# Kernel tuning notes

Hardware: AMD Instinct MI355X
Metric: run time of the kernel (lower is better)

## Reference

```python
import jax, jax.numpy as jnp
import numpy as np

N = 50000      # nodes
E = 800000     # edges (before self-loops)
G = 64         # graphs in batch
IN, HID, OUT, H = 128, 64, 64, 4
NEG_SLOPE = 0.2
BN_EPS = 1e-5


def setup_inputs() -> dict:
    key = jax.random.key(0)
    ks = jax.random.split(key, 16)
    s = 0.1
    return {
        "x": jax.random.normal(ks[0], (N, IN), jnp.float32),
        "edge_index": jax.random.randint(ks[1], (2, E), 0, N, dtype=jnp.int64),
        "batch": jnp.sort(jax.random.randint(ks[2], (N,), 0, G, dtype=jnp.int64)),
        "num_graphs": G,
        "W1": jax.random.normal(ks[3], (IN, H * HID), jnp.float32) * s,
        "att_src1": jax.random.normal(ks[4], (H, HID), jnp.float32) * s,
        "att_dst1": jax.random.normal(ks[5], (H, HID), jnp.float32) * s,
        "b1": jnp.zeros((HID,), jnp.float32),
        "W2": jax.random.normal(ks[6], (HID, H * OUT), jnp.float32) * s,
        "att_src2": jax.random.normal(ks[7], (H, OUT), jnp.float32) * s,
        "att_dst2": jax.random.normal(ks[8], (H, OUT), jnp.float32) * s,
        "b2": jnp.zeros((OUT,), jnp.float32),
        "gate_w1": jax.random.normal(ks[9], (OUT, OUT), jnp.float32) * s,
        "gate_b1": jnp.zeros((OUT,), jnp.float32),
        "bn_gamma": jnp.ones((OUT,), jnp.float32),
        "bn_beta": jnp.zeros((OUT,), jnp.float32),
        "gate_w2": jax.random.normal(ks[10], (OUT, 1), jnp.float32) * s,
        "gate_b2": jnp.zeros((1,), jnp.float32),
        "lin_w": jax.random.normal(ks[11], (OUT, 1), jnp.float32) * s,
        "lin_b": jnp.zeros((1,), jnp.float32),
    }


def segment_softmax(e, seg, num_segments):
    # numerically stable softmax over segments (per-destination / per-graph)
    m = jax.ops.segment_max(e, seg, num_segments=num_segments)
    m = jnp.where(jnp.isfinite(m), m, 0.0)
    ex = jnp.exp(e - m[seg])
    den = jax.ops.segment_sum(ex, seg, num_segments=num_segments)
    return ex / (den[seg] + 1e-16)


def gat_conv(x, src, dst, n, W, a_src, a_dst, b, heads, ch):
    h = (x @ W).reshape(n, heads, ch)                 # [N,H,C]
    asrc = jnp.sum(h * a_src, axis=-1)                # [N,H]
    adst = jnp.sum(h * a_dst, axis=-1)                # [N,H]
    e = jax.nn.leaky_relu(asrc[src] + adst[dst], NEG_SLOPE)   # [E',H]
    alpha = segment_softmax(e, dst, n)                # softmax over incoming edges
    out = jax.ops.segment_sum(h[src] * alpha[:, :, None], dst, num_segments=n)
    return jnp.mean(out, axis=1) + b                  # concat=False -> head mean


def reference(x, edge_index, batch, num_graphs, W1, att_src1, att_dst1, b1,
              W2, att_src2, att_dst2, b2, gate_w1, gate_b1, bn_gamma, bn_beta,
              gate_w2, gate_b2, lin_w, lin_b):
    n = x.shape[0]
    loop = jnp.arange(n, dtype=edge_index.dtype)      # PyG add_self_loops default
    src = jnp.concatenate([edge_index[0], loop])
    dst = jnp.concatenate([edge_index[1], loop])

    out = jax.nn.sigmoid(gat_conv(x, src, dst, n, W1, att_src1, att_dst1, b1, H, HID))
    out = jax.nn.sigmoid(gat_conv(out, src, dst, n, W2, att_src2, att_dst2, b2, H, OUT))

    # GlobalAttention pooling; gate_nn = Linear -> BN(eval, rm=0, rv=1) -> ReLU -> Linear
    g = out @ gate_w1 + gate_b1
    g = (g / jnp.sqrt(1.0 + BN_EPS)) * bn_gamma + bn_beta
    g = jax.nn.relu(g) @ gate_w2 + gate_b2            # [N,1]
    gate = segment_softmax(g, batch, num_graphs)      # per-graph softmax
    pooled = jax.ops.segment_sum(gate * out, batch, num_segments=num_graphs)  # [G,OUT]

    return jax.nn.sigmoid(pooled @ lin_w + lin_b)     # [G,1]
```

## Files before the change

### kernel.cpp

```cpp
#include <hip/hip_runtime.h>


constexpr int NN = 50000;
constexpr int EE = 800000;
constexpr int NG = 64;
constexpr float NEG = 0.2f;
constexpr int MT = NN / 16;
constexpr int SLOTS = 64;
constexpr int CH = 16;
constexpr int GB = (MT + 3) / 4;

constexpr int EB_EDGES = 4096;
constexpr int EBN = (EE + EB_EDGES - 1) / EB_EDGES;
constexpr int NBKT = (NN + 255) / 256;
constexpr int CAP = 48;
constexpr int OVFCAP = 8192;

using bf16x8 = __attribute__((ext_vector_type(8))) __bf16;
using f32x4  = __attribute__((ext_vector_type(4))) float;
using f32x2  = __attribute__((ext_vector_type(2))) float;

__device__ __forceinline__ float wred(float v) {
#pragma unroll
  for (int o = 32; o; o >>= 1) v += __shfl_down(v, o);
  return v;
}
__device__ __forceinline__ float sigmoidf(float v) { return 1.f / (1.f + __expf(-v)); }
__device__ __forceinline__ float lrelu(float v) { return fmaxf(v, NEG * v); }
__device__ __forceinline__ unsigned short f2b(float f) {
  union { float f; unsigned u; } v; v.f = f;
  unsigned r = v.u + 0x7fff + ((v.u >> 16) & 1);
  return (unsigned short)(r >> 16);
}
__device__ __forceinline__ float b2f(unsigned short b) {
  union { unsigned u; float f; } v; v.u = ((unsigned)b) << 16;
  return v.f;
}

__global__ void prep_kernel(const float* __restrict__ W1, const float* __restrict__ W2,
                            const float* __restrict__ gw1, const float* __restrict__ gamma,
                            const int* __restrict__ batch,
                            unsigned short* __restrict__ W1b, unsigned short* __restrict__ W2b,
                            unsigned short* __restrict__ Bg, int* __restrict__ goffs,
                            int* __restrict__ ovf_cnt) {
  int b = blockIdx.x;
  if (b < 128) {
    int idx = b * 256 + threadIdx.x;
    int j = idx & 7, lane = (idx >> 3) & 63, rest = idx >> 9;
    int kc = rest & 3, ntile = rest >> 2;
    W1b[idx] = f2b(W1[(kc * 32 + (lane >> 4) * 8 + j) * 256 + ntile * 16 + (lane & 15)]);
    return;
  }
  if (b < 192) {
    int idx = (b - 128) * 256 + threadIdx.x;
    int j = idx & 7, lane = (idx >> 3) & 63, rest = idx >> 9;
    int kc = rest & 1, ntile = rest >> 1;
    W2b[idx] = f2b(W2[(kc * 32 + (lane >> 4) * 8 + j) * 256 + ntile * 16 + (lane & 15)]);
    return;
  }
  if (b < 208) {
    int idx = (b - 192) * 256 + threadIdx.x;
    int j = idx & 7, lane = (idx >> 3) & 63, rest = idx >> 9;
    int kc = rest & 1, nt = rest >> 1;
    int k = kc * 32 + (lane >> 4) * 8 + j;
    int n = nt * 16 + (lane & 15);
    Bg[idx] = f2b(gw1[k * 64 + n] * gamma[n] * rsqrtf(1.f + 1e-5f));
    return;
  }
  if (threadIdx.x == 0) *ovf_cnt = 0;
  int g = threadIdx.x;
  if (g <= NG) {
    int lo = 0, hi = NN;
    while (lo < hi) {
      int mid = (lo + hi) >> 1;
      if (batch[mid] < g) lo = mid + 1; else hi = mid;
    }
    goffs[g] = lo;
  }
}

template <int K, bool A32>
__device__ __forceinline__ void gemm_body(int mt, int lane,
                                          const void* __restrict__ A_raw,
                                          const unsigned short* __restrict__ Bp,
                                          unsigned char* __restrict__ C8,
                                          const float* __restrict__ att_s,
                                          const float* __restrict__ att_d,
                                          float* __restrict__ asrc,
                                          float* __restrict__ adst) {
  constexpr int KC = K / 32;
  int m0 = mt * 16;
  int q = lane >> 4, r = lane & 15;
  f32x4 acc[16] = {};
#pragma unroll
  for (int kc = 0; kc < KC; ++kc) {
    bf16x8 a;
    if constexpr (A32) {
      const float* Arow = (const float*)A_raw + (size_t)(m0 + r) * K + q * 8 + kc * 32;
      float4 f0 = *(const float4*)Arow;
      float4 f1 = *(const float4*)(Arow + 4);
      union { bf16x8 v; unsigned short s[8]; } u;
      u.s[0] = f2b(f0.x); u.s[1] = f2b(f0.y); u.s[2] = f2b(f0.z); u.s[3] = f2b(f0.w);
      u.s[4] = f2b(f1.x); u.s[5] = f2b(f1.y); u.s[6] = f2b(f1.z); u.s[7] = f2b(f1.w);
      a = u.v;
    } else {
      a = *(const bf16x8*)((const unsigned short*)A_raw +
                           (size_t)(m0 + r) * K + q * 8 + kc * 32);
    }
#pragma unroll
    for (int nt = 0; nt < 16; ++nt) {
      bf16x8 b = *(const bf16x8*)&Bp[(((size_t)nt * KC + kc) * 64 + lane) * 8];
      acc[nt] = __builtin_amdgcn_mfma_f32_16x16x32_bf16(a, b, acc[nt], 0, 0, 0);
    }
  }
#pragma unroll
  for (int nt = 0; nt < 16; ++nt) {
    unsigned col = nt * 16 + r;
#pragma unroll
    for (int reg = 0; reg < 4; ++reg) {
      unsigned row = m0 + q * 4 + reg;
      int p = __builtin_amdgcn_cvt_pk_fp8_f32(acc[nt][reg], 0.f, 0, false);
      C8[row * 256u + col] = (unsigned char)(p & 0xff);
    }
  }
  float ps[4][4] = {}, pd[4][4] = {};
#pragma unroll
  for (int head = 0; head < 4; ++head) {
#pragma unroll
    for (int i = 0; i < 4; ++i) {
      float sv = att_s[head * 64 + i * 16 + r];
      float dv = att_d[head * 64 + i * 16 + r];
#pragma unroll
      for (int reg = 0; reg < 4; ++reg) {
        ps[head][reg] += acc[head * 4 + i][reg] * sv;
        pd[head][reg] += acc[head * 4 + i][reg] * dv;
      }
    }
  }
#pragma unroll
  for (int head = 0; head < 4; ++head)
#pragma unroll
    for (int reg = 0; reg < 4; ++reg)
#pragma unroll
      for (int o = 1; o < 16; o <<= 1) {
        ps[head][reg] += __shfl_xor(ps[head][reg], o);
        pd[head][reg] += __shfl_xor(pd[head][reg], o);
      }
  if (r == 0) {
#pragma unroll
    for (int reg = 0; reg < 4; ++reg) {
      int row = m0 + q * 4 + reg;
#pragma unroll
      for (int head = 0; head < 4; ++head) {
        asrc[row * 4 + head] = ps[head][reg];
        adst[row * 4 + head] = pd[head][reg];
      }
    }
  }
}

__global__ void gemm1_build_kernel(const float* __restrict__ x,
                                   const unsigned short* __restrict__ W1b,
                                   unsigned char* __restrict__ C8,
                                   const float* __restrict__ att_s,
                                   const float* __restrict__ att_d,
                                   float* __restrict__ asrc, float* __restrict__ adst,
                                   const int* __restrict__ ei,
                                   unsigned* __restrict__ bins,
                                   int* __restrict__ binCnt,
                                   int* __restrict__ ovf_cnt,
                                   unsigned* __restrict__ ovf) {
  int b = blockIdx.x;
  if (b < GB) {
    int wave = threadIdx.x >> 6, lane = threadIdx.x & 63;
    int mt = b * 4 + wave;
    if (mt >= MT) return;
    gemm_body<128, true>(mt, lane, x, W1b, C8, att_s, att_d, asrc, adst);
    return;
  }
  int hb = b - GB;
  __shared__ int hist[NBKT];
  for (int t = threadIdx.x; t < NBKT; t += 256) hist[t] = 0;
  __syncthreads();
  int e0 = hb * EB_EDGES + threadIdx.x * 16;
#pragma unroll
  for (int k4 = 0; k4 < 4; ++k4) {
    int e = e0 + k4 * 4;
    if (e >= EE) break;
    int4 s4 = *(const int4*)&ei[e];
    int4 d4 = *(const int4*)&ei[EE + e];
    int ss[4] = {s4.x, s4.y, s4.z, s4.w};
    int dd[4] = {d4.x, d4.y, d4.z, d4.w};
#pragma unroll
    for (int u = 0; u < 4; ++u) {
      if (e + u >= EE) break;
      int src = ss[u], dst = dd[u];
      int bkt = dst >> 8;
      int r = atomicAdd(&hist[bkt], 1);
      if (r < CAP) {
        bins[((unsigned)hb * NBKT + bkt) * CAP + r] =
            (unsigned)src | ((unsigned)(dst & 255) << 16);
      } else {
        int o = atomicAdd(ovf_cnt, 1);
        if (o < OVFCAP) ovf[o] = (unsigned)src | ((unsigned)dst << 16);
      }
    }
  }
  __syncthreads();
  for (int t = threadIdx.x; t < NBKT; t += 256) binCnt[hb * NBKT + t] = hist[t];
}

__global__ __launch_bounds__(1024) void csr_build_kernel(
    const unsigned* __restrict__ bins, const int* __restrict__ binCnt,
    const int* __restrict__ ovf_cnt, const unsigned* __restrict__ ovf,
    unsigned short* __restrict__ csr16, int* __restrict__ cnt) {
  int b = blockIdx.x;
  __shared__ int hist[256];
  int t = threadIdx.x;
  int node0 = b << 8;
  if (t < 256) {
    hist[t] = 1;
    int node = node0 + t;
    if (node < NN) csr16[(unsigned)node * SLOTS] = (unsigned short)node;
  }
  __syncthreads();
  int wave = t >> 6, lane = t & 63;
  for (int i = wave; i < EBN; i += 16) {
    int c = binCnt[i * NBKT + b];
    if (c > CAP) c = CAP;
    for (int base = 0; base < c; base += 64) {
      int j = base + lane;
      if (j < c) {
        unsigned p = bins[((unsigned)i * NBKT + b) * CAP + j];
        int dl = p >> 16, src = p & 0xffff;
        int r = atomicAdd(&hist[dl], 1);
        if (r < SLOTS) csr16[(unsigned)(node0 + dl) * SLOTS + r] = (unsigned short)src;
      }
    }
  }
  __syncthreads();
  int oc = *ovf_cnt;
  if (oc > OVFCAP) oc = OVFCAP;
  for (int j = t; j < oc; j += 1024) {
    unsigned p = ovf[j];
    int dst = (int)(p >> 16);
    if ((dst >> 8) == b) {
      int r = atomicAdd(&hist[dst & 255], 1);
      if (r < SLOTS) csr16[(unsigned)dst * SLOTS + r] = (unsigned short)(p & 0xffff);
    }
  }
  __syncthreads();
  if (t < 256) {
    int node = node0 + t;
    if (node < NN) cnt[node] = hist[t];
  }
}

__global__ void aggregate_kernel(const unsigned char* __restrict__ h8,
                                 const float* __restrict__ asrc,
                                 const float* __restrict__ adst,
                                 const int* __restrict__ cnt,
                                 const unsigned short* __restrict__ csr_src,
                                 const float* __restrict__ bias,
                                 unsigned short* __restrict__ outb) {
  int wave = threadIdx.x >> 6, lane = threadIdx.x & 63;
  int node = blockIdx.x * 4 + wave;
  if (node >= NN) return;
  int deg = min(cnt[node], SLOTS);
  int hgrp = lane >> 4;
  int hb = lane & 48;
  float adh = adst[node * 4 + hgrp];
  int src_all = csr_src[(unsigned)node * SLOTS + lane];
  float wreg[4];
  float den = 0.f;
#pragma unroll
  for (int i = 0; i < 4; ++i) {
    int slot = i * 16 + (lane & 15);
    int s = __shfl(src_all, slot);
    bool valid = slot < deg;
    float xv = asrc[(unsigned)(valid ? s : 0) * 4 + hgrp];
    float w = __expf(lrelu(xv + adh));
    wreg[i] = valid ? w : 0.f;
    den += wreg[i];
  }
#pragma unroll
  for (int o = 1; o < 16; o <<= 1) den += __shfl_xor(den, o);
  const unsigned char* hp = h8 + (unsigned)lane * 4;
  f32x2 a01 = {0.f, 0.f}, a23 = {0.f, 0.f};
  int e = 0;
#pragma unroll
  for (int i = 0; i < 4; ++i) {
    if (e >= deg) break;
    float wcur = wreg[i];
    int bound = min(deg, (i + 1) * 16);
    for (; e + 3 < bound; e += 4) {
      int s0 = __shfl(src_all, e),     s1 = __shfl(src_all, e + 1);
      int s2 = __shfl(src_all, e + 2), s3 = __shfl(src_all, e + 3);
      float w0 = __shfl(wcur, ((e)     & 15) | hb);
      float w1 = __shfl(wcur, ((e + 1) & 15) | hb);
      float w2 = __shfl(wcur, ((e + 2) & 15) | hb);
      float w3 = __shfl(wcur, ((e + 3) & 15) | hb);
      unsigned d0 = *(const unsigned*)(hp + ((unsigned)s0 << 8));
      unsigned d1 = *(const unsigned*)(hp + ((unsigned)s1 << 8));
      unsigned d2 = *(const unsigned*)(hp + ((unsigned)s2 << 8));
      unsigned d3 = *(const unsigned*)(hp + ((unsigned)s3 << 8));
      f32x2 l0 = __builtin_amdgcn_cvt_pk_f32_fp8(d0, false), u0 = __builtin_amdgcn_cvt_pk_f32_fp8(d0, true);
      f32x2 l1 = __builtin_amdgcn_cvt_pk_f32_fp8(d1, false), u1 = __builtin_amdgcn_cvt_pk_f32_fp8(d1, true);
      f32x2 l2 = __builtin_amdgcn_cvt_pk_f32_fp8(d2, false), u2 = __builtin_amdgcn_cvt_pk_f32_fp8(d2, true);
      f32x2 l3 = __builtin_amdgcn_cvt_pk_f32_fp8(d3, false), u3 = __builtin_amdgcn_cvt_pk_f32_fp8(d3, true);
      a01 += l0 * w0; a23 += u0 * w0;
      a01 += l1 * w1; a23 += u1 * w1;
      a01 += l2 * w2; a23 += u2 * w2;
      a01 += l3 * w3; a23 += u3 * w3;
    }
    for (; e < bound; ++e) {
      int s0 = __shfl(src_all, e);
      float w0 = __shfl(wcur, (e & 15) | hb);
      unsigned d0 = *(const unsigned*)(hp + ((unsigned)s0 << 8));
      f32x2 l0 = __builtin_amdgcn_cvt_pk_f32_fp8(d0, false), u0 = __builtin_amdgcn_cvt_pk_f32_fp8(d0, true);
      a01 += l0 * w0; a23 += u0 * w0;
    }
  }
  float inv = 1.f / (den + 1e-16f);
  float r0 = a01.x * inv, r1 = a01.y * inv, r2 = a23.x * inv, r3 = a23.y * inv;
  r0 += __shfl_xor(r0, 16); r0 += __shfl_xor(r0, 32);
  r1 += __shfl_xor(r1, 16); r1 += __shfl_xor(r1, 32);
  r2 += __shfl_xor(r2, 16); r2 += __shfl_xor(r2, 32);
  r3 += __shfl_xor(r3, 16); r3 += __shfl_xor(r3, 32);
  if (lane < 16) {
    float4 bv = *(const float4*)&bias[lane * 4];
    ushort4 o;
    o.x = f2b(sigmoidf(0.25f * r0 + bv.x));
    o.y = f2b(sigmoidf(0.25f * r1 + bv.y));
    o.z = f2b(sigmoidf(0.25f * r2 + bv.z));
    o.w = f2b(sigmoidf(0.25f * r3 + bv.w));
    *(ushort4*)&outb[(size_t)node * 64 + lane * 4] = o;
  }
}

__global__ void gemm2_kernel(const unsigned short* __restrict__ out1b,
                             const unsigned short* __restrict__ W2b,
                             unsigned char* __restrict__ C8,
                             const float* __restrict__ att_s,
                             const float* __restrict__ att_d,
                             float* __restrict__ asrc, float* __restrict__ adst) {
  int wave = threadIdx.x >> 6, lane = threadIdx.x & 63;
  int mt = blockIdx.x * 4 + wave;
  if (mt >= MT) return;
  gemm_body<64, false>(mt, lane, out1b, W2b, C8, att_s, att_d, asrc, adst);
}

__global__ void pool_partial_kernel(const int* __restrict__ goffs,
                                    const unsigned short* __restrict__ out2b,
                                    const unsigned short* __restrict__ Bg,
                                    const float* __restrict__ gb1,
                                    const float* __restrict__ gamma,
                                    const float* __restrict__ beta,
                                    const float* __restrict__ gw2,
                                    const float* __restrict__ gb2,
                                    float* __restrict__ part_acc,
                                    float* __restrict__ part_den) {
  int b = blockIdx.x, j = blockIdx.y;
  int beg = goffs[b], end = goffs[b + 1];
  int chunk = (end - beg + CH - 1) / CH;
  int cb = beg + j * chunk;
  int ce = min(end, cb + chunk);
  int lane = threadIdx.x & 63, wave = threadIdx.x >> 6;
  int q = lane >> 4, r = lane & 15;
  const float s = rsqrtf(1.f + 1e-5f);
  float gb2v = gb2[0];
  float accv = 0.f, den = 0.f;
  for (int n0 = cb + wave * 16; n0 < ce; n0 += 64) {
    f32x4 acc[4] = {};
    int row = n0 + r;
    if (row >= NN) row = NN - 1;
    const unsigned short* Arow = out2b + (size_t)row * 64 + q * 8;
#pragma unroll
    for (int kc = 0; kc < 2; ++kc) {
      bf16x8 a = *(const bf16x8*)(Arow + kc * 32);
#pragma unroll
      for (int nt = 0; nt < 4; ++nt) {
        bf16x8 b8 = *(const bf16x8*)&Bg[(((size_t)nt * 2 + kc) * 64 + lane) * 8];
        acc[nt] = __builtin_amdgcn_mfma_f32_16x16x32_bf16(a, b8, acc[nt], 0, 0, 0);
      }
    }
    float sum[4] = {0.f, 0.f, 0.f, 0.f};
#pragma unroll
    for (int nt = 0; nt < 4; ++nt) {
      int col = nt * 16 + r;
      float off = gb1[col] * gamma[col] * s + beta[col];
      float w2 = gw2[col];
#pragma unroll
      for (int reg = 0; reg < 4; ++reg)
        sum[reg] += fmaxf(acc[nt][reg] + off, 0.f) * w2;
    }
#pragma unroll
    for (int reg = 0; reg < 4; ++reg)
#pragma unroll
      for (int o = 1; o < 16; o <<= 1) sum[reg] += __shfl_xor(sum[reg], o);
    float gx[4];
#pragma unroll
    for (int reg = 0; reg < 4; ++reg) {
      int n = n0 + q * 4 + reg;
      gx[reg] = (n < ce) ? __expf(sum[reg] + gb2v) : 0.f;
    }
#pragma unroll
    for (int t = 0; t < 16; ++t) {
      int n = n0 + t;
      if (n >= ce) break;
      float gv = __shfl(gx[t & 3], (t >> 2) << 4);
      accv += gv * b2f(out2b[(size_t)n * 64 + lane]);
      den += gv;
    }
  }
  __shared__ float sacc[4][64];
  __shared__ float sden[4];
  sacc[wave][lane] = accv;
  if (lane == 0) sden[wave] = den;
  __syncthreads();
  if (wave == 0) {
    float a = sacc[0][lane] + sacc[1][lane] + sacc[2][lane] + sacc[3][lane];
    part_acc[((size_t)b * CH + j) * 64 + lane] = a;
    if (lane == 0) part_den[b * CH + j] = sden[0] + sden[1] + sden[2] + sden[3];
  }
}

__global__ void pool_final_kernel(const float* __restrict__ part_acc,
                                  const float* __restrict__ part_den,
                                  const float* __restrict__ lw, const float* __restrict__ lb,
                                  float* __restrict__ out) {
  int b = blockIdx.x, lane = threadIdx.x;
  float a = 0.f;
#pragma unroll
  for (int j = 0; j < CH; ++j) a += part_acc[((size_t)b * CH + j) * 64 + lane];
  float den = (lane < CH) ? part_den[b * CH + lane] : 0.f;
  den = wred(den);
  den = __shfl(den, 0);
  float p = a / (den + 1e-16f);
  float v = wred(p * lw[lane]);
  if (lane == 0) out[b] = sigmoidf(v + lb[0]);
}

extern "C" void kernel_launch(void* const* d_in, const int* in_sizes, int n_in,
                              void* d_out, int out_size, void* d_ws, size_t ws_size,
                              hipStream_t stream) {
  const float* x    = (const float*)d_in[0];
  const int*   ei   = (const int*)d_in[1];
  const int*   batch= (const int*)d_in[2];
  const float* W1   = (const float*)d_in[4];
  const float* as1  = (const float*)d_in[5];
  const float* ad1  = (const float*)d_in[6];
  const float* b1   = (const float*)d_in[7];
  const float* W2   = (const float*)d_in[8];
  const float* as2  = (const float*)d_in[9];
  const float* ad2  = (const float*)d_in[10];
  const float* b2   = (const float*)d_in[11];
  const float* gw1  = (const float*)d_in[12];
  const float* gb1  = (const float*)d_in[13];
  const float* gamma= (const float*)d_in[14];
  const float* beta = (const float*)d_in[15];
  const float* gw2  = (const float*)d_in[16];
  const float* gb2  = (const float*)d_in[17];
  const float* lw   = (const float*)d_in[18];
  const float* lb   = (const float*)d_in[19];
  float* out = (float*)d_out;

  char* ws = (char*)d_ws;
  size_t off = 0;
  auto alloc = [&](size_t bytes) -> void* {
    void* p = ws + off;
    off = (off + bytes + 255) & ~(size_t)255;
    return p;
  };
  unsigned short* W1b    = (unsigned short*)alloc((size_t)128 * 256 * 2);
  unsigned short* W2b    = (unsigned short*)alloc((size_t)64 * 256 * 2);
  unsigned short* Bg     = (unsigned short*)alloc((size_t)64 * 64 * 2);
  unsigned char*  h8     = (unsigned char*)alloc((size_t)NN * 256);
  unsigned short* out1b  = (unsigned short*)alloc((size_t)NN * 64 * 2);
  unsigned short* out2b  = (unsigned short*)alloc((size_t)NN * 64 * 2);
  float*    asrc    = (float*)alloc((size_t)NN * 4 * 4);
  float*    adst    = (float*)alloc((size_t)NN * 4 * 4);
  int*      cnt     = (int*)alloc((size_t)NN * 4);
  unsigned short* csr16 = (unsigned short*)alloc((size_t)NN * SLOTS * 2);
  unsigned* bins    = (unsigned*)alloc((size_t)EBN * NBKT * CAP * 4);
  int*      binCnt  = (int*)alloc((size_t)EBN * NBKT * 4);
  int*      ovf_cnt = (int*)alloc(256);
  unsigned* ovf     = (unsigned*)alloc((size_t)OVFCAP * 4);
  int*      goffs   = (int*)alloc((size_t)(NG + 1) * 4);
  float*    pacc    = (float*)alloc((size_t)NG * CH * 64 * 4);
  float*    pden    = (float*)alloc((size_t)NG * CH * 4);

  const int nodeBlocks = (NN + 3) / 4;

  prep_kernel<<<209, 256, 0, stream>>>(W1, W2, gw1, gamma, batch,
                                       W1b, W2b, Bg, goffs, ovf_cnt);

  gemm1_build_kernel<<<GB + EBN, 256, 0, stream>>>(x, W1b, h8, as1, ad1, asrc, adst,
                                                   ei, bins, binCnt, ovf_cnt, ovf);
  csr_build_kernel<<<NBKT, 1024, 0, stream>>>(bins, binCnt, ovf_cnt, ovf, csr16, cnt);

  aggregate_kernel<<<nodeBlocks, 256, 0, stream>>>(h8, asrc, adst, cnt, csr16, b1, out1b);

  gemm2_kernel<<<GB, 256, 0, stream>>>(out1b, W2b, h8, as2, ad2, asrc, adst);
  aggregate_kernel<<<nodeBlocks, 256, 0, stream>>>(h8, asrc, adst, cnt, csr16, b2, out2b);

  pool_partial_kernel<<<dim3(NG, CH), 256, 0, stream>>>(goffs, out2b, Bg, gb1, gamma, beta,
                                                        gw2, gb2, pacc, pden);
  pool_final_kernel<<<NG, 64, 0, stream>>>(pacc, pden, lw, lb, out);
}
```

Before: 257.1 us.

## Gather 16-byte fp8 rows per lane across four edges with LDS reduction

Reworks the GAT aggregation kernel so each group of 16 lanes loads a full 256-byte fp8 neighbour row with 16-byte vector loads. The four lane quarters each process a different edge at the same time, instead of every lane loading 4 bytes per edge in sequence. Partial sums are combined across quarters and heads through a shared-memory reduction behind a block barrier, and each lane writes one output channel. The aim is fewer, wider gather loads and more memory-level parallelism, at the cost of more accumulator registers, LDS traffic and a __syncthreads. The early-exit guard is removed on the assumption that the node count divides by 4.

Result: faster. 248.8 us (-3.2%).

```diff
diff --git a/kernel.cpp b/kernel.cpp
--- a/kernel.cpp
+++ b/kernel.cpp
@@ -15,6 +15,8 @@
 constexpr int NBKT = (NN + 255) / 256;
 constexpr int CAP = 48;
 constexpr int OVFCAP = 8192;
+
+static_assert(NN % 4 == 0, "aggregate barrier assumes no early-exit waves");
 
 using bf16x8 = __attribute__((ext_vector_type(8))) __bf16;
 using f32x4  = __attribute__((ext_vector_type(4))) float;
@@ -265,17 +267,18 @@
                                  unsigned short* __restrict__ outb) {
   int wave = threadIdx.x >> 6, lane = threadIdx.x & 63;
   int node = blockIdx.x * 4 + wave;
-  if (node >= NN) return;
   int deg = min(cnt[node], SLOTS);
   int hgrp = lane >> 4;
-  int hb = lane & 48;
+  int q4 = lane >> 4;
+  int r16 = lane & 15;
+  int hbase = (r16 >> 2) << 4;
   float adh = adst[node * 4 + hgrp];
   int src_all = csr_src[(unsigned)node * SLOTS + lane];
   float wreg[4];
   float den = 0.f;
 #pragma unroll
   for (int i = 0; i < 4; ++i) {
-    int slot = i * 16 + (lane & 15);
+    int slot = i * 16 + r16;
     int s = __shfl(src_all, slot);
     bool valid = slot < deg;
     float xv = asrc[(unsigned)(valid ? s : 0) * 4 + hgrp];
@@ -285,57 +288,78 @@
   }
 #pragma unroll
   for (int o = 1; o < 16; o <<= 1) den += __shfl_xor(den, o);
-  const unsigned char* hp = h8 + (unsigned)lane * 4;
-  f32x2 a01 = {0.f, 0.f}, a23 = {0.f, 0.f};
+
+  const unsigned char* hp = h8 + (unsigned)r16 * 16;
+  f32x2 a[8] = {};
+#define ACC4(d, wv)                                                         \
+  {                                                                         \
+    a[0] += __builtin_amdgcn_cvt_pk_f32_fp8((d).x, false) * (wv);           \
+    a[1] += __builtin_amdgcn_cvt_pk_f32_fp8((d).x, true) * (wv);            \
+    a[2] += __builtin_amdgcn_cvt_pk_f32_fp8((d).y, false) * (wv);           \
+    a[3] += __builtin_amdgcn_cvt_pk_f32_fp8((d).y, true) * (wv);            \
+    a[4] += __builtin_amdgcn_cvt_pk_f32_fp8((d).z, false) * (wv);           \
+    a[5] += __builtin_amdgcn_cvt_pk_f32_fp8((d).z, true) * (wv);            \
+    a[6] += __builtin_amdgcn_cvt_pk_f32_fp8((d).w, false) * (wv);           \
+    a[7] += __builtin_amdgcn_cvt_pk_f32_fp8((d).w, true) * (wv);            \
+  }
   int e = 0;
 #pragma unroll
   for (int i = 0; i < 4; ++i) {
     if (e >= deg) break;
     float wcur = wreg[i];
     int bound = min(deg, (i + 1) * 16);
-    for (; e + 3 < bound; e += 4) {
-      int s0 = __shfl(src_all, e),     s1 = __shfl(src_all, e + 1);
-      int s2 = __shfl(src_all, e + 2), s3 = __shfl(src_all, e + 3);
-      float w0 = __shfl(wcur, ((e)     & 15) | hb);
-      float w1 = __shfl(wcur, ((e + 1) & 15) | hb);
-      float w2 = __shfl(wcur, ((e + 2) & 15) | hb);
-      float w3 = __shfl(wcur, ((e + 3) & 15) | hb);
-      unsigned d0 = *(const unsigned*)(hp + ((unsigned)s0 << 8));
-      unsigned d1 = *(const unsigned*)(hp + ((unsigned)s1 << 8));
-      unsigned d2 = *(const unsigned*)(hp + ((unsigned)s2 << 8));
-      unsigned d3 = *(const unsigned*)(hp + ((unsigned)s3 << 8));
-      f32x2 l0 = __builtin_amdgcn_cvt_pk_f32_fp8(d0, false), u0 = __builtin_amdgcn_cvt_pk_f32_fp8(d0, true);
-      f32x2 l1 = __builtin_amdgcn_cvt_pk_f32_fp8(d1, false), u1 = __builtin_amdgcn_cvt_pk_f32_fp8(d1, true);
-      f32x2 l2 = __builtin_amdgcn_cvt_pk_f32_fp8(d2, false), u2 = __builtin_amdgcn_cvt_pk_f32_fp8(d2, true);
-      f32x2 l3 = __builtin_amdgcn_cvt_pk_f32_fp8(d3, false), u3 = __builtin_amdgcn_cvt_pk_f32_fp8(d3, true);
-      a01 += l0 * w0; a23 += u0 * w0;
-      a01 += l1 * w1; a23 += u1 * w1;
-      a01 += l2 * w2; a23 += u2 * w2;
-      a01 += l3 * w3; a23 += u3 * w3;
-    }
-    for (; e < bound; ++e) {
-      int s0 = __shfl(src_all, e);
-      float w0 = __shfl(wcur, (e & 15) | hb);
-      unsigned d0 = *(const unsigned*)(hp + ((unsigned)s0 << 8));
-      f32x2 l0 = __builtin_amdgcn_cvt_pk_f32_fp8(d0, false), u0 = __builtin_amdgcn_cvt_pk_f32_fp8(d0, true);
-      a01 += l0 * w0; a23 += u0 * w0;
-    }
-  }
-  float inv = 1.f / (den + 1e-16f);
-  float r0 = a01.x * inv, r1 = a01.y * inv, r2 = a23.x * inv, r3 = a23.y * inv;
-  r0 += __shfl_xor(r0, 16); r0 += __shfl_xor(r0, 32);
-  r1 += __shfl_xor(r1, 16); r1 += __shfl_xor(r1, 32);
-  r2 += __shfl_xor(r2, 16); r2 += __shfl_xor(r2, 32);
-  r3 += __shfl_xor(r3, 16); r3 += __shfl_xor(r3, 32);
-  if (lane < 16) {
-    float4 bv = *(const float4*)&bias[lane * 4];
-    ushort4 o;
-    o.x = f2b(sigmoidf(0.25f * r0 + bv.x));
-    o.y = f2b(sigmoidf(0.25f * r1 + bv.y));
-    o.z = f2b(sigmoidf(0.25f * r2 + bv.z));
-    o.w = f2b(sigmoidf(0.25f * r3 + bv.w));
-    *(ushort4*)&outb[(size_t)node * 64 + lane * 4] = o;
-  }
+    if (bound - e == 16) {
+      int eq = e + q4, wq = hbase + q4;
+      int s0 = __shfl(src_all, eq);
+      int s1 = __shfl(src_all, eq + 4);
+      int s2 = __shfl(src_all, eq + 8);
+      int s3 = __shfl(src_all, eq + 12);
+      float w0 = __shfl(wcur, wq);
+      float w1 = __shfl(wcur, wq + 4);
+      float w2 = __shfl(wcur, wq + 8);
+      float w3 = __shfl(wcur, wq + 12);
+      uint4 d0 = *(const uint4*)(hp + ((unsigned)s0 << 8));
+      uint4 d1 = *(const uint4*)(hp + ((unsigned)s1 << 8));
+      uint4 d2 = *(const uint4*)(hp + ((unsigned)s2 << 8));
+      uint4 d3 = *(const uint4*)(hp + ((unsigned)s3 << 8));
+      ACC4(d0, w0); ACC4(d1, w1); ACC4(d2, w2); ACC4(d3, w3);
+      e += 16;
+    } else {
+      for (; e < bound; e += 4) {
+        int gg = min(4, bound - e);
+        int q4e = min(q4, gg - 1);
+        int su = __shfl(src_all, e + q4e);
+        float wv = __shfl(wcur, hbase + (e & 15) + q4e);
+        if (q4 >= gg) wv = 0.f;
+        uint4 d = *(const uint4*)(hp + ((unsigned)su << 8));
+        ACC4(d, wv);
+      }
+    }
+  }
+#undef ACC4
+  float den2 = __shfl(den, (r16 >> 2) << 4);
+  float inv = 0.25f / (den2 + 1e-16f);
+  __shared__ float red[4][1024];
+  float* wb = &red[wave][(unsigned)lane * 16];
+  f32x4 v0 = {a[0].x * inv, a[0].y * inv, a[1].x * inv, a[1].y * inv};
+  f32x4 v1 = {a[2].x * inv, a[2].y * inv, a[3].x * inv, a[3].y * inv};
+  f32x4 v2 = {a[4].x * inv, a[4].y * inv, a[5].x * inv, a[5].y * inv};
+  f32x4 v3 = {a[6].x * inv, a[6].y * inv, a[7].x * inv, a[7].y * inv};
+  *(f32x4*)(wb + 0) = v0;
+  *(f32x4*)(wb + 4) = v1;
+  *(f32x4*)(wb + 8) = v2;
+  *(f32x4*)(wb + 12) = v3;
+  __syncthreads();
+  const float* rb = &red[wave][0];
+  int vbase = (lane >> 4) * 16 + (lane & 15);
+  float s = 0.f;
+#pragma unroll
+  for (int q = 0; q < 4; ++q)
+#pragma unroll
+    for (int h = 0; h < 4; ++h)
+      s += rb[vbase + q * 256 + h * 64];
+  float ov = sigmoidf(s + bias[lane]);
+  outb[(size_t)node * 64 + lane] = f2b(ov);
 }
 
 __global__ void gemm2_kernel(const unsigned short* __restrict__ out1b,
@@ -490,7 +514,7 @@
   float*    pacc    = (float*)alloc((size_t)NG * CH * 64 * 4);
   float*    pden    = (float*)alloc((size_t)NG * CH * 4);
 
-  const int nodeBlocks = (NN + 3) / 4;
+  const int nodeBlocks = NN / 4;
 
   prep_kernel<<<209, 256, 0, stream>>>(W1, W2, gw1, gamma, batch,
                                        W1b, W2b, Bg, goffs, ovf_cnt);
```
